# Kernel optimization log

Hardware: AMD Instinct MI355X
Metric: run time of the kernel (lower is better)

Reference implementation:

```python
import jax, jax.numpy as jnp
import numpy as np

N_AE = 512
N_DE = 256
N = 100000
NUM_SEG = 1024
EPS = 1e-5


def setup_inputs() -> dict:
    key = jax.random.key(0)
    ks = jax.random.split(key, 20)
    d_in1 = 2 * N_AE + N_DE  # 1280
    inp = {
        "x": jax.random.normal(ks[0], (N, 2 * N_AE), dtype=jnp.float32),
        "dist_feat": jax.random.normal(ks[1], (N, N_DE), dtype=jnp.float32),
        "atom_idx": jax.random.randint(ks[2], (N,), 0, 100, dtype=jnp.int32),
        "ele_idx": jax.random.randint(ks[3], (N,), 0, NUM_SEG, dtype=jnp.int32),
        # layer 1 params
        "l1_w": jax.random.normal(ks[4], (d_in1, N_AE), dtype=jnp.float32) * (1.0 / np.sqrt(d_in1)),
        "l1_b": jnp.zeros((N_AE,), dtype=jnp.float32),
        "l1_g": jnp.ones((N_AE,), dtype=jnp.float32),
        "l1_be": jnp.zeros((N_AE,), dtype=jnp.float32),
        # layer 2 params (same input width: 2*n_ae + n_de)
        "l2_w": jax.random.normal(ks[5], (d_in1, N_AE), dtype=jnp.float32) * (1.0 / np.sqrt(d_in1)),
        "l2_b": jnp.zeros((N_AE,), dtype=jnp.float32),
        "l2_g": jnp.ones((N_AE,), dtype=jnp.float32),
        "l2_be": jnp.zeros((N_AE,), dtype=jnp.float32),
        # final fc + bn
        "f_w": jax.random.normal(ks[6], (2 * N_AE, N_AE), dtype=jnp.float32) * (1.0 / np.sqrt(2 * N_AE)),
        "f_b": jnp.zeros((N_AE,), dtype=jnp.float32),
        "f_g": jnp.ones((N_AE,), dtype=jnp.float32),
        "f_be": jnp.zeros((N_AE,), dtype=jnp.float32),
    }
    return inp


def _bn(h, gamma, beta):
    # BatchNorm1d in training mode: batch stats, biased variance
    m = jnp.mean(h, axis=0)
    v = jnp.mean(jnp.square(h - m), axis=0)
    return gamma * (h - m) * jax.lax.rsqrt(v + EPS) + beta


def _dist_layer(x_cat, ele_idx, w, b, gamma, beta):
    h = jax.nn.relu(_bn(x_cat @ w + b, gamma, beta))  # [N, n_ae]
    sums = jax.ops.segment_sum(h, ele_idx, num_segments=NUM_SEG)  # [S, n_ae]
    cnt = jax.ops.segment_sum(jnp.ones((h.shape[0],), h.dtype), ele_idx, num_segments=NUM_SEG)
    mean = sums / jnp.maximum(cnt, 1.0)[:, None]
    return jnp.concatenate([h, mean[ele_idx]], axis=1)  # [N, 2*n_ae]


def reference(x, dist_feat, atom_idx, ele_idx,
              l1_w, l1_b, l1_g, l1_be,
              l2_w, l2_b, l2_g, l2_be,
              f_w, f_b, f_g, f_be):
    h = _dist_layer(jnp.concatenate([x, dist_feat], axis=1), ele_idx, l1_w, l1_b, l1_g, l1_be)
    h = _dist_layer(jnp.concatenate([h, dist_feat], axis=1), ele_idx, l2_w, l2_b, l2_g, l2_be)
    out = jax.nn.relu(_bn(h @ f_w + f_b, f_g, f_be))  # [N, n_ae]
    return out
```

## Files before the change

kernel.cpp:

```cpp
#include <hip/hip_runtime.h>
#include <stdint.h>
#include <stdio.h>

#define NOUT 512
#define NSEG 1024

typedef unsigned short u16;
typedef __attribute__((ext_vector_type(4))) float f32x4;
typedef __attribute__((ext_vector_type(8))) short s16x8;
typedef __attribute__((ext_vector_type(4))) unsigned short u16x4;

__device__ __forceinline__ u16 f2b(float f) {
  union { float f; uint32_t u; } v; v.f = f;
  uint32_t r = v.u + 0x7FFFu + ((v.u >> 16) & 1u);
  return (u16)(r >> 16);
}
__device__ __forceinline__ float b2f(u16 b) {
  union { uint32_t u; float f; } v; v.u = ((uint32_t)b) << 16;
  return v.f;
}

typedef __attribute__((address_space(1))) const void GAS;
typedef __attribute__((address_space(3))) void LAS;
__device__ __forceinline__ void llds16(const void* g, void* l) {
  __builtin_amdgcn_global_load_lds((GAS*)g, (LAS*)l, 16, 0, 0);
}

__global__ void k_cast(const float* __restrict__ src, u16* __restrict__ dst, long n4) {
  long i = blockIdx.x * (long)blockDim.x + threadIdx.x;
  long stride = (long)gridDim.x * blockDim.x;
  for (; i < n4; i += stride) {
    float4 v = reinterpret_cast<const float4*>(src)[i];
    u16x4 o;
    o.x = f2b(v.x); o.y = f2b(v.y); o.z = f2b(v.z); o.w = f2b(v.w);
    reinterpret_cast<u16x4*>(dst)[i] = o;
  }
}

__global__ void k_wtcastT(const float* __restrict__ w, u16* __restrict__ out, int K) {
  __shared__ float tile[32][33];
  int k0 = blockIdx.x * 32, c0 = blockIdx.y * 32;
  int t = threadIdx.x;
  int rr = t >> 5, cc = t & 31;
#pragma unroll
  for (int p = 0; p < 4; ++p)
    tile[p * 8 + rr][cc] = w[(long)(k0 + p * 8 + rr) * NOUT + c0 + cc];
  __syncthreads();
#pragma unroll
  for (int p = 0; p < 4; ++p)
    out[(long)(c0 + p * 8 + rr) * K + k0 + cc] = f2b(tile[cc][p * 8 + rr]);
}

__global__ void k_hist(const int* __restrict__ ele, int* __restrict__ cnt, int N) {
  int i = blockIdx.x * blockDim.x + threadIdx.x;
  int stride = gridDim.x * blockDim.x;
  for (; i < N; i += stride) atomicAdd(&cnt[ele[i]], 1);
}

__global__ void k_scan(const int* __restrict__ cnt, int* __restrict__ off) {
  __shared__ int tmp[NSEG];
  int t = threadIdx.x;
  tmp[t] = cnt[t];
  __syncthreads();
  for (int o = 1; o < NSEG; o <<= 1) {
    int add = (t >= o) ? tmp[t - o] : 0;
    __syncthreads();
    tmp[t] += add;
    __syncthreads();
  }
  off[t] = tmp[t] - cnt[t];
}

__global__ void k_scatter(const int* __restrict__ ele, const int* __restrict__ off,
                          int* __restrict__ fill, int* __restrict__ rows, int N) {
  int i = blockIdx.x * blockDim.x + threadIdx.x;
  int stride = gridDim.x * blockDim.x;
  for (; i < N; i += stride) {
    int e = ele[i];
    int p = atomicAdd(&fill[e], 1);
    rows[off[e] + p] = i;
  }
}

__global__ void k_finalize(const float* __restrict__ sum, const float* __restrict__ sumsq,
                           const float* __restrict__ g, const float* __restrict__ be,
                           float* __restrict__ A, float* __restrict__ C, int M) {
  int c = threadIdx.x;
  float m = sum[c] / (float)M;
  float v = sumsq[c] / (float)M - m * m;
  float a = g[c] * rsqrtf(v + 1e-5f);
  A[c] = a;
  C[c] = be[c] - a * m;
}

__global__ void k_bnseg(const u16* __restrict__ hp, u16* __restrict__ h, u16* __restrict__ mean,
                        const float* __restrict__ A, const float* __restrict__ C,
                        const int* __restrict__ off, const int* __restrict__ cnt,
                        const int* __restrict__ rows) {
  int s = blockIdx.x;
  int c0 = blockIdx.y * 128 + 2 * threadIdx.x;
  int n = cnt[s], o = off[s];
  float a0 = A[c0], a1 = A[c0 + 1], cc0 = C[c0], cc1 = C[c0 + 1];
  float s0 = 0.f, s1 = 0.f;
  for (int j = 0; j < n; ++j) {
    int r = rows[o + j];
    uint32_t v = *reinterpret_cast<const uint32_t*>(&hp[(long)r * NOUT + c0]);
    float h0 = fmaxf(a0 * b2f((u16)(v & 0xffff)) + cc0, 0.f);
    float h1 = fmaxf(a1 * b2f((u16)(v >> 16)) + cc1, 0.f);
    s0 += h0; s1 += h1;
    *reinterpret_cast<uint32_t*>(&h[(long)r * NOUT + c0]) =
        ((uint32_t)f2b(h1) << 16) | (uint32_t)f2b(h0);
  }
  float inv = 1.f / fmaxf((float)n, 1.f);
  *reinterpret_cast<uint32_t*>(&mean[(long)s * NOUT + c0]) =
      ((uint32_t)f2b(s1 * inv) << 16) | (uint32_t)f2b(s0 * inv);
}

__global__ void k_final(const u16* __restrict__ hp, float* __restrict__ out,
                        const float* __restrict__ A, const float* __restrict__ C, long n4) {
  long i = blockIdx.x * (long)blockDim.x + threadIdx.x;
  long stride = (long)gridDim.x * blockDim.x;
  for (; i < n4; i += stride) {
    u16x4 v = reinterpret_cast<const u16x4*>(hp)[i];
    int c0 = (int)((i * 4) & (NOUT - 1));
    float4 a = *reinterpret_cast<const float4*>(&A[c0]);
    float4 c = *reinterpret_cast<const float4*>(&C[c0]);
    float4 o;
    o.x = fmaxf(a.x * b2f(v.x) + c.x, 0.f);
    o.y = fmaxf(a.y * b2f(v.y) + c.y, 0.f);
    o.z = fmaxf(a.z * b2f(v.z) + c.z, 0.f);
    o.w = fmaxf(a.w * b2f(v.w) + c.w, 0.f);
    reinterpret_cast<float4*>(out)[i] = o;
  }
}

__global__ __launch_bounds__(256, 3) void k_gemm(
    const u16* p0, const u16* p1, int e0, int w0, int w1, int g0, int g1,
    const int* __restrict__ ele,
    const u16* __restrict__ wbt, int ldb, int e0b, int bskip,
    const float* __restrict__ tab, int addtab,
    u16* __restrict__ outp, float* __restrict__ outf, int wf32,
    float* __restrict__ csum, float* __restrict__ csq, int dostats,
    int M, int K) {
  __shared__ __align__(16) u16 As[2 * 4096];
  __shared__ __align__(16) u16 Bs[2 * 4096];

  int nwg = gridDim.x;
  int orig = blockIdx.x;
  int q = nwg >> 3, r8 = nwg & 7;
  int xcd = orig & 7, loc = orig >> 3;
  int bid = (xcd < r8 ? xcd * (q + 1) : r8 * (q + 1) + (xcd - r8) * q) + loc;
  int mt = bid >> 2, ct = bid & 3;
  int brow = mt * 128, bcol = ct * 128;

  int tid = (int)threadIdx.x;
  int lane = tid & 63;
  int wid = tid >> 6;
  int wr = wid >> 1, wc = wid & 1;
  int l15 = lane & 15, kg = lane >> 4;

  int srow = tid >> 2;
  int soct = ((tid & 3) ^ ((srow >> 1) & 3)) * 8;

  int gr0 = brow + srow, gr1 = gr0 + 64;
  int gr0c = gr0 < M ? gr0 : M - 1;
  int gr1c = gr1 < M ? gr1 : M - 1;
  int el0 = ele[gr0c], el1 = ele[gr1c];

  const u16* a00 = p0 + (long)(g0 ? el0 : gr0c) * w0 + soct;
  const u16* a01 = p1 + (long)(g1 ? el0 : gr0c) * w1 + soct - e0;
  const u16* a10 = p0 + (long)(g0 ? el1 : gr1c) * w0 + soct;
  const u16* a11 = p1 + (long)(g1 ? el1 : gr1c) * w1 + soct - e0;

  const u16* b0p = wbt + (long)(bcol + srow) * ldb + soct;
  const u16* b1p = wbt + (long)(bcol + srow + 64) * ldb + soct;

  int xoct = (kg ^ ((l15 >> 1) & 3)) * 8;
  int aro = (wr * 64 + l15) * 32 + xoct;
  int bro = (wc * 64 + l15) * 32 + xoct;

  f32x4 acc[4][4];
#pragma unroll
  for (int m = 0; m < 4; ++m)
#pragma unroll
    for (int n = 0; n < 4; ++n)
#pragma unroll
      for (int j = 0; j < 4; ++j) acc[m][n][j] = 0.f;

  int KT = K >> 5;
  int dst = wid * 512;

  auto stage = [&](int tt, int buf) {
    int k0 = tt << 5;
    const u16* sa0 = k0 < e0 ? a00 : a01;
    const u16* sa1 = k0 < e0 ? a10 : a11;
    int bo = k0 + (k0 >= e0b ? bskip : 0);
    int ab = buf * 4096 + dst;
    llds16(sa0 + k0, &As[ab]);
    llds16(sa1 + k0, &As[ab + 2048]);
    llds16(b0p + bo, &Bs[ab]);
    llds16(b1p + bo, &Bs[ab + 2048]);
  };

  stage(0, 0);
  __syncthreads();

  for (int t = 0; t < KT; ++t) {
    int cur = t & 1;
    if (t + 1 < KT) stage(t + 1, cur ^ 1);
    __builtin_amdgcn_sched_barrier(0);
    const u16* Ab = &As[cur * 4096];
    const u16* Bb = &Bs[cur * 4096];
    s16x8 af[4], bf[4];
#pragma unroll
    for (int m = 0; m < 4; ++m)
      af[m] = *reinterpret_cast<const s16x8*>(&Ab[m * 512 + aro]);
#pragma unroll
    for (int n = 0; n < 4; ++n)
      bf[n] = *reinterpret_cast<const s16x8*>(&Bb[n * 512 + bro]);
#pragma unroll
    for (int m = 0; m < 4; ++m)
#pragma unroll
      for (int n = 0; n < 4; ++n)
        acc[m][n] = __builtin_amdgcn_mfma_f32_16x16x32_bf16(af[m], bf[n], acc[m][n], 0, 0, 0);
    __syncthreads();
  }

  float sums[4] = {0.f, 0.f, 0.f, 0.f}, sqs[4] = {0.f, 0.f, 0.f, 0.f};
#pragma unroll
  for (int m = 0; m < 4; ++m) {
    int row0 = brow + wr * 64 + m * 16 + kg * 4;
#pragma unroll
    for (int j = 0; j < 4; ++j) {
      int r = row0 + j;
      if (r < M) {
        long rb = (long)r * NOUT;
        long tb = addtab ? (long)ele[r] * NOUT : 0;
#pragma unroll
        for (int n = 0; n < 4; ++n) {
          int col = bcol + wc * 64 + n * 16 + l15;
          float v = acc[m][n][j];
          if (addtab) v += tab[tb + col];
          if (wf32) outf[rb + col] = v;
          else outp[rb + col] = f2b(v);
          sums[n] += v;
          sqs[n] += v * v;
        }
      }
    }
  }
  if (dostats) {
#pragma unroll
    for (int n = 0; n < 4; ++n) {
      sums[n] += __shfl_xor(sums[n], 16);
      sums[n] += __shfl_xor(sums[n], 32);
      sqs[n] += __shfl_xor(sqs[n], 16);
      sqs[n] += __shfl_xor(sqs[n], 32);
    }
    if (kg == 0) {
#pragma unroll
      for (int n = 0; n < 4; ++n) {
        int col = bcol + wc * 64 + n * 16 + l15;
        atomicAdd(&csum[col], sums[n]);
        atomicAdd(&csq[col], sqs[n]);
      }
    }
  }
}

extern "C" void kernel_launch(void* const* d_in, const int* in_sizes, int n_in,
                              void* d_out, int out_size, void* d_ws, size_t ws_size,
                              hipStream_t stream) {
  const float* x    = (const float*)d_in[0];
  const float* dist = (const float*)d_in[1];
  const int* ele    = (const int*)d_in[3];
  const float* l1w  = (const float*)d_in[4];
  const float* l1g  = (const float*)d_in[6];
  const float* l1be = (const float*)d_in[7];
  const float* l2w  = (const float*)d_in[8];
  const float* l2g  = (const float*)d_in[10];
  const float* l2be = (const float*)d_in[11];
  const float* fw   = (const float*)d_in[12];
  const float* fg   = (const float*)d_in[14];
  const float* fbe  = (const float*)d_in[15];

  int N = in_sizes[0] / 1024;
  float* out = (float*)d_out;
  u16* xbf = (u16*)d_out;

  int MT = (N + 127) / 128;

  char* w = (char*)d_ws;
  auto alloc = [&](size_t bytes) {
    char* p = w;
    w += (bytes + 255) & ~(size_t)255;
    return p;
  };
  u16* dist_bf = (u16*)alloc((size_t)N * 256 * 2);
  u16* hp      = (u16*)alloc((size_t)N * NOUT * 2);
  u16* h       = (u16*)alloc((size_t)N * NOUT * 2);
  u16* mean    = (u16*)alloc((size_t)NSEG * NOUT * 2);
  u16* w1bt    = (u16*)alloc((size_t)NOUT * 1280 * 2);
  u16* w2bt    = (u16*)alloc((size_t)NOUT * 1280 * 2);
  u16* fbt     = (u16*)alloc((size_t)NOUT * 1024 * 2);
  float* mc2   = (float*)alloc((size_t)NSEG * NOUT * 4);
  float* mc3   = (float*)alloc((size_t)NSEG * NOUT * 4);
  float* colsum = (float*)alloc(NOUT * 4 * 2);
  float* colsumsq = colsum + NOUT;
  float* bnA   = (float*)alloc(NOUT * 4);
  float* bnC   = (float*)alloc(NOUT * 4);
  int* seg_cnt = (int*)alloc(NSEG * 4);
  int* seg_off = (int*)alloc(NSEG * 4);
  int* seg_fill = (int*)alloc(NSEG * 4);
  int* rows    = (int*)alloc((size_t)N * 4);

  size_t need = (size_t)(w - (char*)d_ws);
  if (need > ws_size) {
    fprintf(stderr, "kernel_launch: ws too small: need %zu have %zu\n", need, ws_size);
    return;
  }

  long n4x = (long)N * 1024 / 4;
  long n4d = (long)N * 256 / 4;
  long n4h = (long)N * NOUT / 4;
  int gemmGrid = MT * 4;
  int mcGrid = (NSEG / 128) * 4;
  dim3 bnsegGrid(NSEG, 4);

  k_cast<<<4096, 256, 0, stream>>>(x, xbf, n4x);
  k_cast<<<2048, 256, 0, stream>>>(dist, dist_bf, n4d);
  dim3 wt1(1280 / 32, 16), wt3(1024 / 32, 16);
  k_wtcastT<<<wt1, 256, 0, stream>>>(l1w, w1bt, 1280);
  k_wtcastT<<<wt1, 256, 0, stream>>>(l2w, w2bt, 1280);
  k_wtcastT<<<wt3, 256, 0, stream>>>(fw, fbt, 1024);

  hipMemsetAsync(seg_cnt, 0, NSEG * 4, stream);
  hipMemsetAsync(seg_fill, 0, NSEG * 4, stream);
  k_hist<<<512, 256, 0, stream>>>(ele, seg_cnt, N);
  k_scan<<<1, NSEG, 0, stream>>>(seg_cnt, seg_off);
  k_scatter<<<512, 256, 0, stream>>>(ele, seg_off, seg_fill, rows, N);

  hipMemsetAsync(colsum, 0, NOUT * 4 * 2, stream);
  k_gemm<<<gemmGrid, 256, 0, stream>>>(xbf, dist_bf, 1024, 1024, 256, 0, 0, ele,
                                       w1bt, 1280, 1280, 0, mc2, 0,
                                       hp, mc2, 0, colsum, colsumsq, 1, N, 1280);
  k_finalize<<<1, NOUT, 0, stream>>>(colsum, colsumsq, l1g, l1be, bnA, bnC, N);
  k_bnseg<<<bnsegGrid, 64, 0, stream>>>(hp, h, mean, bnA, bnC, seg_off, seg_cnt, rows);

  k_gemm<<<mcGrid, 256, 0, stream>>>(mean, mean, 512, 512, 512, 0, 0, ele,
                                     w2bt + 512, 1280, 512, 0, mc2, 0,
                                     hp, mc2, 1, colsum, colsumsq, 0, NSEG, 512);
  hipMemsetAsync(colsum, 0, NOUT * 4 * 2, stream);
  k_gemm<<<gemmGrid, 256, 0, stream>>>(h, dist_bf, 512, 512, 256, 0, 0, ele,
                                       w2bt, 1280, 512, 512, mc2, 1,
                                       hp, mc2, 0, colsum, colsumsq, 1, N, 768);
  k_finalize<<<1, NOUT, 0, stream>>>(colsum, colsumsq, l2g, l2be, bnA, bnC, N);
  k_bnseg<<<bnsegGrid, 64, 0, stream>>>(hp, h, mean, bnA, bnC, seg_off, seg_cnt, rows);

  k_gemm<<<mcGrid, 256, 0, stream>>>(mean, mean, 512, 512, 512, 0, 0, ele,
                                     fbt + 512, 1024, 512, 0, mc3, 0,
                                     hp, mc3, 1, colsum, colsumsq, 0, NSEG, 512);
  hipMemsetAsync(colsum, 0, NOUT * 4 * 2, stream);
  k_gemm<<<gemmGrid, 256, 0, stream>>>(h, h, 512, 512, 512, 0, 0, ele,
                                       fbt, 1024, 512, 0, mc3, 1,
                                       hp, mc3, 0, colsum, colsumsq, 1, N, 512);
  k_finalize<<<1, NOUT, 0, stream>>>(colsum, colsumsq, fg, fbe, bnA, bnC, N);
  k_final<<<4096, 256, 0, stream>>>(hp, out, bnA, bnC, n4h);
}
```

Before: 988.3 us.

## Load GEMM fragments directly from global memory and template K dimensions

The GEMM kernel no longer stages A and B tiles through double-buffered shared memory with global_load_lds. Each lane instead loads its MFMA fragments directly from global memory into registers, and the loop is fully unrolled via template parameters for K and the concatenation offsets. This removes LDS traffic and per-iteration barriers. In exchange, data is no longer reused across waves in a block, global/L2 reads increase, and register pressure grows from the unrolled loads.

```diff
diff --git a/kernel.cpp b/kernel.cpp
--- a/kernel.cpp
+++ b/kernel.cpp
@@ -18,12 +18,6 @@
 __device__ __forceinline__ float b2f(u16 b) {
   union { uint32_t u; float f; } v; v.u = ((uint32_t)b) << 16;
   return v.f;
-}
-
-typedef __attribute__((address_space(1))) const void GAS;
-typedef __attribute__((address_space(3))) void LAS;
-__device__ __forceinline__ void llds16(const void* g, void* l) {
-  __builtin_amdgcn_global_load_lds((GAS*)g, (LAS*)l, 16, 0, 0);
 }
 
 __global__ void k_cast(const float* __restrict__ src, u16* __restrict__ dst, long n4) {
@@ -134,17 +128,15 @@
   }
 }
 
+template <int K, int E0, int W0, int W1, int G0, int G1, int E0B, int BSKIP>
 __global__ __launch_bounds__(256, 3) void k_gemm(
-    const u16* p0, const u16* p1, int e0, int w0, int w1, int g0, int g1,
+    const u16* __restrict__ p0, const u16* __restrict__ p1,
     const int* __restrict__ ele,
-    const u16* __restrict__ wbt, int ldb, int e0b, int bskip,
+    const u16* __restrict__ wbt, int ldb,
     const float* __restrict__ tab, int addtab,
     u16* __restrict__ outp, float* __restrict__ outf, int wf32,
     float* __restrict__ csum, float* __restrict__ csq, int dostats,
-    int M, int K) {
-  __shared__ __align__(16) u16 As[2 * 4096];
-  __shared__ __align__(16) u16 Bs[2 * 4096];
-
+    int M) {
   int nwg = gridDim.x;
   int orig = blockIdx.x;
   int q = nwg >> 3, r8 = nwg & 7;
@@ -159,25 +151,22 @@
   int wr = wid >> 1, wc = wid & 1;
   int l15 = lane & 15, kg = lane >> 4;
 
-  int srow = tid >> 2;
-  int soct = ((tid & 3) ^ ((srow >> 1) & 3)) * 8;
-
-  int gr0 = brow + srow, gr1 = gr0 + 64;
-  int gr0c = gr0 < M ? gr0 : M - 1;
-  int gr1c = gr1 < M ? gr1 : M - 1;
-  int el0 = ele[gr0c], el1 = ele[gr1c];
-
-  const u16* a00 = p0 + (long)(g0 ? el0 : gr0c) * w0 + soct;
-  const u16* a01 = p1 + (long)(g1 ? el0 : gr0c) * w1 + soct - e0;
-  const u16* a10 = p0 + (long)(g0 ? el1 : gr1c) * w0 + soct;
-  const u16* a11 = p1 + (long)(g1 ? el1 : gr1c) * w1 + soct - e0;
-
-  const u16* b0p = wbt + (long)(bcol + srow) * ldb + soct;
-  const u16* b1p = wbt + (long)(bcol + srow + 64) * ldb + soct;
-
-  int xoct = (kg ^ ((l15 >> 1) & 3)) * 8;
-  int aro = (wr * 64 + l15) * 32 + xoct;
-  int bro = (wc * 64 + l15) * 32 + xoct;
+  const char* cp0 = (const char*)p0;
+  const char* cp1 = (const char*)p1;
+  const char* cpb = (const char*)wbt;
+
+  uint32_t va0[4], va1[4], vb[4];
+#pragma unroll
+  for (int m = 0; m < 4; ++m) {
+    int r = brow + wr * 64 + m * 16 + l15;
+    if (r >= M) r = M - 1;
+    int e = (G0 | G1) ? ele[r] : 0;
+    va0[m] = (uint32_t)((G0 ? e : r) * W0 + kg * 8) * 2u;
+    va1[m] = (uint32_t)((G1 ? e : r) * W1 + kg * 8) * 2u;
+  }
+#pragma unroll
+  for (int n = 0; n < 4; ++n)
+    vb[n] = (uint32_t)((bcol + wc * 64 + n * 16 + l15) * ldb + kg * 8) * 2u;
 
   f32x4 acc[4][4];
 #pragma unroll
@@ -187,43 +176,26 @@
 #pragma unroll
       for (int j = 0; j < 4; ++j) acc[m][n][j] = 0.f;
 
-  int KT = K >> 5;
-  int dst = wid * 512;
-
-  auto stage = [&](int tt, int buf) {
-    int k0 = tt << 5;
-    const u16* sa0 = k0 < e0 ? a00 : a01;
-    const u16* sa1 = k0 < e0 ? a10 : a11;
-    int bo = k0 + (k0 >= e0b ? bskip : 0);
-    int ab = buf * 4096 + dst;
-    llds16(sa0 + k0, &As[ab]);
-    llds16(sa1 + k0, &As[ab + 2048]);
-    llds16(b0p + bo, &Bs[ab]);
-    llds16(b1p + bo, &Bs[ab + 2048]);
-  };
-
-  stage(0, 0);
-  __syncthreads();
-
-  for (int t = 0; t < KT; ++t) {
-    int cur = t & 1;
-    if (t + 1 < KT) stage(t + 1, cur ^ 1);
-    __builtin_amdgcn_sched_barrier(0);
-    const u16* Ab = &As[cur * 4096];
-    const u16* Bb = &Bs[cur * 4096];
+#pragma unroll
+  for (int t = 0; t < K / 32; ++t) {
+    const int k0 = t * 32;
     s16x8 af[4], bf[4];
 #pragma unroll
-    for (int m = 0; m < 4; ++m)
-      af[m] = *reinterpret_cast<const s16x8*>(&Ab[m * 512 + aro]);
+    for (int m = 0; m < 4; ++m) {
+      if (k0 < E0)
+        af[m] = *reinterpret_cast<const s16x8*>(cp0 + va0[m] + 2 * k0);
+      else
+        af[m] = *reinterpret_cast<const s16x8*>(cp1 + va1[m] + 2 * (k0 - E0));
+    }
+    const int bo = k0 + (k0 >= E0B ? BSKIP : 0);
 #pragma unroll
     for (int n = 0; n < 4; ++n)
-      bf[n] = *reinterpret_cast<const s16x8*>(&Bb[n * 512 + bro]);
+      bf[n] = *reinterpret_cast<const s16x8*>(cpb + vb[n] + 2 * bo);
 #pragma unroll
     for (int m = 0; m < 4; ++m)
 #pragma unroll
       for (int n = 0; n < 4; ++n)
         acc[m][n] = __builtin_amdgcn_mfma_f32_16x16x32_bf16(af[m], bf[n], acc[m][n], 0, 0, 0);
-    __syncthreads();
   }
 
   float sums[4] = {0.f, 0.f, 0.f, 0.f}, sqs[4] = {0.f, 0.f, 0.f, 0.f};
@@ -341,29 +313,24 @@
   k_scatter<<<512, 256, 0, stream>>>(ele, seg_off, seg_fill, rows, N);
 
   hipMemsetAsync(colsum, 0, NOUT * 4 * 2, stream);
-  k_gemm<<<gemmGrid, 256, 0, stream>>>(xbf, dist_bf, 1024, 1024, 256, 0, 0, ele,
-                                       w1bt, 1280, 1280, 0, mc2, 0,
-                                       hp, mc2, 0, colsum, colsumsq, 1, N, 1280);
+  k_gemm<1280, 1024, 1024, 256, 0, 0, 1280, 0><<<gemmGrid, 256, 0, stream>>>(
+      xbf, dist_bf, ele, w1bt, 1280, mc2, 0, hp, mc2, 0, colsum, colsumsq, 1, N);
   k_finalize<<<1, NOUT, 0, stream>>>(colsum, colsumsq, l1g, l1be, bnA, bnC, N);
   k_bnseg<<<bnsegGrid, 64, 0, stream>>>(hp, h, mean, bnA, bnC, seg_off, seg_cnt, rows);
 
-  k_gemm<<<mcGrid, 256, 0, stream>>>(mean, mean, 512, 512, 512, 0, 0, ele,
-                                     w2bt + 512, 1280, 512, 0, mc2, 0,
-                                     hp, mc2, 1, colsum, colsumsq, 0, NSEG, 512);
+  k_gemm<512, 512, 512, 512, 0, 0, 512, 0><<<mcGrid, 256, 0, stream>>>(
+      mean, mean, ele, w2bt + 512, 1280, mc2, 0, hp, mc2, 1, colsum, colsumsq, 0, NSEG);
   hipMemsetAsync(colsum, 0, NOUT * 4 * 2, stream);
-  k_gemm<<<gemmGrid, 256, 0, stream>>>(h, dist_bf, 512, 512, 256, 0, 0, ele,
-                                       w2bt, 1280, 512, 512, mc2, 1,
-                                       hp, mc2, 0, colsum, colsumsq, 1, N, 768);
+  k_gemm<768, 512, 512, 256, 0, 0, 512, 512><<<gemmGrid, 256, 0, stream>>>(
+      h, dist_bf, ele, w2bt, 1280, mc2, 1, hp, mc2, 0, colsum, colsumsq, 1, N);
   k_finalize<<<1, NOUT, 0, stream>>>(colsum, colsumsq, l2g, l2be, bnA, bnC, N);
   k_bnseg<<<bnsegGrid, 64, 0, stream>>>(hp, h, mean, bnA, bnC, seg_off, seg_cnt, rows);
 
-  k_gemm<<<mcGrid, 256, 0, stream>>>(mean, mean, 512, 512, 512, 0, 0, ele,
-                                     fbt + 512, 1024, 512, 0, mc3, 0,
-                                     hp, mc3, 1, colsum, colsumsq, 0, NSEG, 512);
+  k_gemm<512, 512, 512, 512, 0, 0, 512, 0><<<mcGrid, 256, 0, stream>>>(
+      mean, mean, ele, fbt + 512, 1024, mc3, 0, hp, mc3, 1, colsum, colsumsq, 0, NSEG);
   hipMemsetAsync(colsum, 0, NOUT * 4 * 2, stream);
-  k_gemm<<<gemmGrid, 256, 0, stream>>>(h, h, 512, 512, 512, 0, 0, ele,
-                                       fbt, 1024, 512, 0, mc3, 1,
-                                       hp, mc3, 0, colsum, colsumsq, 1, N, 512);
+  k_gemm<512, 512, 512, 512, 0, 0, 512, 0><<<gemmGrid, 256, 0, stream>>>(
+      h, h, ele, fbt, 1024, mc3, 1, hp, mc3, 0, colsum, colsumsq, 1, N);
   k_finalize<<<1, NOUT, 0, stream>>>(colsum, colsumsq, fg, fbe, bnA, bnC, N);
   k_final<<<4096, 256, 0, stream>>>(hp, out, bnA, bnC, n4h);
 }
```

Result: slower. 1.586 ms (+60.5%).
